# Performance work log

Hardware: AMD Instinct MI355X
Metric: run time of the kernel (lower is better)

Reference implementation:

```python
import jax, jax.numpy as jnp
import numpy as np

H = 512
V = 50000
S = 400
B = 64


def setup_inputs() -> dict:
    key = jax.random.key(0)
    ks = jax.random.split(key, 20)
    inp = {
        'input': jax.random.normal(ks[0], (1, B, H), jnp.float32),
        'encoder_states': jax.random.normal(ks[1], (S, B, H), jnp.float32),
        'oov_enc_mask': jax.random.randint(ks[2], (S, B), 0, 2, jnp.int32),
        'hidden': jnp.zeros((1, B, H), jnp.float32),
        # GRU params (PyTorch layout: gates ordered r, z, n)
        'W_ih': jax.random.normal(ks[3], (3 * H, H), jnp.float32) * 0.02,
        'W_hh': jax.random.normal(ks[4], (3 * H, H), jnp.float32) * 0.02,
        'b_ih': jax.random.normal(ks[5], (3 * H,), jnp.float32) * 0.02,
        'b_hh': jax.random.normal(ks[6], (3 * H,), jnp.float32) * 0.02,
        # output vocab projection Linear(2H, V)
        'out_W': jax.random.normal(ks[7], (V, 2 * H), jnp.float32) * 0.02,
        'out_b': jax.random.normal(ks[8], (V,), jnp.float32) * 0.02,
        # additive attention params
        'v': jax.random.normal(ks[9], (H, 1), jnp.float32) * 0.02,
        'Wh': jax.random.normal(ks[10], (H, H), jnp.float32) * 0.02,
        'Ws': jax.random.normal(ks[11], (H, H), jnp.float32) * 0.02,
        'b_attn': jax.random.normal(ks[12], (1, H), jnp.float32) * 0.02,
        # pointer probability Linears (H -> 1)
        'pWh': jax.random.normal(ks[13], (1, H), jnp.float32) * 0.02,
        'pWs': jax.random.normal(ks[14], (1, H), jnp.float32) * 0.02,
        'pWx': jax.random.normal(ks[15], (1, H), jnp.float32) * 0.02,
        'pWx_b': jax.random.normal(ks[16], (1,), jnp.float32) * 0.02,
    }
    return inp


def reference(input, encoder_states, oov_enc_mask, hidden,
              W_ih, W_hh, b_ih, b_hh, out_W, out_b,
              v, Wh, Ws, b_attn, pWh, pWs, pWx, pWx_b):
    x = input[0]            # (B, H)
    h0 = hidden[0]          # (B, H)

    # --- single-step GRU (PyTorch gate order r, z, n) ---
    gi = x @ W_ih.T + b_ih      # (B, 3H)
    gh = h0 @ W_hh.T + b_hh     # (B, 3H)
    ir, iz, inn = jnp.split(gi, 3, axis=1)
    hr, hz, hn = jnp.split(gh, 3, axis=1)
    r = jax.nn.sigmoid(ir + hr)
    z = jax.nn.sigmoid(iz + hz)
    n = jnp.tanh(inn + r * hn)
    h = (1.0 - z) * n + z * h0          # decoder_state, (B, H)
    hidden_new = h[None]                # (1, B, H)

    # --- Bahdanau additive attention, softmax over seq axis ---
    x1 = jnp.einsum('sbh,hk->sbk', encoder_states, Wh)   # (S, B, H)
    x2 = h @ Ws                                          # (B, H) broadcasts over S
    scores = jnp.squeeze(jnp.tanh(x1 + x2 + b_attn) @ v, 2)  # (S, B)
    attn = jax.nn.softmax(scores, axis=0)                # (S, B)
    attn_bs = attn.T                                     # (B, S)

    context = jnp.einsum('bs,sbh->bh', attn_bs, encoder_states)  # (B, H)
    global_state = jnp.concatenate([h, context], axis=1)         # (B, 2H)

    # --- pointer probability ---
    p = jax.nn.sigmoid(context @ pWh.T + h @ pWs.T + x @ pWx.T + pWx_b)  # (B, 1)

    vocab_distr = p * jax.nn.selu(global_state @ out_W.T + out_b)        # (B, V)
    oov_vocab_distr = (1.0 - p) * (attn_bs * oov_enc_mask.astype(jnp.float32).T)  # (B, S)
    extended_vocab_distr = jnp.concatenate([vocab_distr, oov_vocab_distr], axis=1)

    return extended_vocab_distr, hidden_new, jnp.squeeze(p), attn
```

## Files before the change

kernel.cpp:

```cpp
#include <hip/hip_runtime.h>
#include <cmath>

#define H    512
#define H2   1024
#define V    50000
#define SEQ  400
#define EXT  (V + SEQ)
#define NB_V 782

typedef __attribute__((ext_vector_type(8))) short short8;
typedef __attribute__((ext_vector_type(4))) float floatx4;

__device__ __forceinline__ unsigned int bfpack2(float lo, float hi) {
    unsigned int a = __float_as_uint(lo) + 0x8000u;
    unsigned int b = __float_as_uint(hi) + 0x8000u;
    return __builtin_amdgcn_perm(b, a, 0x07060302);
}
__device__ __forceinline__ uint4 pack8(float4 a, float4 b) {
    uint4 r;
    r.x = bfpack2(a.x, a.y);
    r.y = bfpack2(a.z, a.w);
    r.z = bfpack2(b.x, b.y);
    r.w = bfpack2(b.z, b.w);
    return r;
}
__device__ __forceinline__ float4 ld4(const float* p) { return *(const float4*)p; }

__global__ __launch_bounds__(256) void k01_fused(
    const float* __restrict__ x, const float* __restrict__ h0,
    const float* __restrict__ W_ih, const float* __restrict__ W_hh,
    float* __restrict__ gacc,
    const float* __restrict__ Wh, const float* __restrict__ Ws,
    unsigned short* __restrict__ WhT, unsigned short* __restrict__ WsT)
{
    __shared__ __align__(16) unsigned char smem[65536];
    const int tid = threadIdx.x;

    if (blockIdx.x >= 64) {
        float (*T)[65] = (float (*)[65])smem;
        const int e   = blockIdx.x - 64;
        const int zz  = e >> 6, rem = e & 63;
        const int k0  = (rem & 7) * 64, n0 = (rem >> 3) * 64;
        const float* src = zz ? Ws : Wh;
        unsigned short* dst = zz ? WsT : WhT;
        #pragma unroll
        for (int i = 0; i < 16; ++i) {
            int ee = i * 256 + tid;
            int r = ee >> 6, c = ee & 63;
            T[r][c] = src[(size_t)(k0 + r) * H + n0 + c];
        }
        __syncthreads();
        #pragma unroll
        for (int i = 0; i < 16; ++i) {
            int ee = i * 256 + tid;
            int nn = ee >> 6, kk = ee & 63;
            unsigned int u = __float_as_uint(T[kk][nn]) + 0x8000u;
            dst[(size_t)(n0 + nn) * H + k0 + kk] = (unsigned short)(u >> 16);
        }
        return;
    }

    uint4* Ax = (uint4*)smem;
    uint4* Ah = (uint4*)(smem + 8192);
    uint4 (*Bg)[512] = (uint4 (*)[512])(smem + 16384);
    const int wave = tid >> 6, lane = tid & 63;
    const int lrow = lane & 15, q = lane >> 4;
    const int jb = blockIdx.x & 7, ks = blockIdx.x >> 3;
    const int J0 = jb * 64;
    const int kc = ks * 64;

    #pragma unroll
    for (int c = 0; c < 2; ++c) {
        int idx = c * 256 + tid;
        int m = idx >> 3, j2 = idx & 7, k8 = j2 ^ (m & 7);
        const float* sx = x  + m * H + kc + k8 * 8;
        const float* sh = h0 + m * H + kc + k8 * 8;
        Ax[idx] = pack8(ld4(sx), ld4(sx + 4));
        Ah[idx] = pack8(ld4(sh), ld4(sh + 4));
    }
    #pragma unroll
    for (int g = 0; g < 6; ++g) {
        const float* Wb = (g < 3) ? W_ih : W_hh;
        const int go = (g % 3) * H;
        #pragma unroll
        for (int c = 0; c < 2; ++c) {
            int idx = c * 256 + tid;
            int n = idx >> 3, j2 = idx & 7, k8 = j2 ^ (n & 7);
            const float* sw = Wb + (size_t)(go + J0 + n) * H + kc + k8 * 8;
            Bg[g][idx] = pack8(ld4(sw), ld4(sw + 4));
        }
    }
    __syncthreads();

    floatx4 accm[6][4];
    #pragma unroll
    for (int g = 0; g < 6; ++g)
        #pragma unroll
        for (int mt = 0; mt < 4; ++mt) accm[g][mt] = (floatx4){0.f, 0.f, 0.f, 0.f};

    #pragma unroll
    for (int kk8 = 0; kk8 < 8; kk8 += 4) {
        const int k8 = kk8 + q;
        short8 ax[4], ah[4];
        #pragma unroll
        for (int mt = 0; mt < 4; ++mt) {
            int m = mt * 16 + lrow;
            ax[mt] = *(const short8*)&Ax[m * 8 + (k8 ^ (m & 7))];
            ah[mt] = *(const short8*)&Ah[m * 8 + (k8 ^ (m & 7))];
        }
        const int n = wave * 16 + lrow;
        const int gidx = n * 8 + (k8 ^ (n & 7));
        #pragma unroll
        for (int g = 0; g < 6; ++g) {
            short8 bb = *(const short8*)&Bg[g][gidx];
            #pragma unroll
            for (int mt = 0; mt < 4; ++mt)
                accm[g][mt] = __builtin_amdgcn_mfma_f32_16x16x32_bf16(
                    (g < 3) ? ax[mt] : ah[mt], bb, accm[g][mt], 0, 0, 0);
        }
    }
    const int j = J0 + wave * 16 + lrow;
    #pragma unroll
    for (int g = 0; g < 6; ++g)
        #pragma unroll
        for (int mt = 0; mt < 4; ++mt)
            #pragma unroll
            for (int r = 0; r < 4; ++r) {
                const int bb = mt * 16 + q * 4 + r;
                gacc[(((size_t)g * 8 + ks) * 64 + bb) * H + j] = accm[g][mt][r];
            }
}

__global__ __launch_bounds__(256) void k1_gru_fin(
    const float* __restrict__ gacc, const float* __restrict__ h0,
    const float* __restrict__ b_ih, const float* __restrict__ b_hh,
    float* __restrict__ h_out)
{
    const int e = blockIdx.x * 256 + threadIdx.x;
    const int j = e & (H - 1);
    const int b = e >> 9;
    float gs[6];
    #pragma unroll
    for (int g = 0; g < 6; ++g) {
        float sum = 0.f;
        #pragma unroll
        for (int ks = 0; ks < 8; ++ks)
            sum += gacc[(((size_t)g * 8 + ks) * 64 + b) * H + j];
        gs[g] = sum;
    }
    float rg = 1.f / (1.f + expf(-(gs[0] + b_ih[j] + gs[3] + b_hh[j])));
    float zg = 1.f / (1.f + expf(-(gs[1] + b_ih[H + j] + gs[4] + b_hh[H + j])));
    float ng = tanhf(gs[2] + b_ih[2 * H + j] + rg * (gs[5] + b_hh[2 * H + j]));
    float h0v = h0[b * H + j];
    h_out[b * H + j] = (1.f - zg) * ng + zg * h0v;
}

__global__ __launch_bounds__(256) void k2_x2(
    const float* __restrict__ h, const unsigned short* __restrict__ WsT,
    const float* __restrict__ b_attn, float* __restrict__ x2)
{
    __shared__ uint4 Ag[512];
    __shared__ uint4 Bgg[512];
    const int tid  = threadIdx.x;
    const int wave = tid >> 6, lane = tid & 63;
    const int lrow = lane & 15, q = lane >> 4;
    const int n0   = blockIdx.x * 64;

    floatx4 acc[4];
    #pragma unroll
    for (int mt = 0; mt < 4; ++mt) acc[mt] = (floatx4){0.f, 0.f, 0.f, 0.f};

    for (int kc = 0; kc < H; kc += 64) {
        __syncthreads();
        #pragma unroll
        for (int c = 0; c < 2; ++c) {
            int idx = c * 256 + tid;
            int m = idx >> 3, j2 = idx & 7, k8 = j2 ^ (m & 7);
            const float* sh = h + m * H + kc + k8 * 8;
            Ag[idx] = pack8(ld4(sh), ld4(sh + 4));
            Bgg[idx] = *(const uint4*)(WsT + (size_t)(n0 + m) * H + kc + k8 * 8);
        }
        __syncthreads();
        #pragma unroll
        for (int kk8 = 0; kk8 < 8; kk8 += 4) {
            const int k8 = kk8 + q;
            const int n = wave * 16 + lrow;
            short8 bb = *(const short8*)&Bgg[n * 8 + (k8 ^ (n & 7))];
            #pragma unroll
            for (int mt = 0; mt < 4; ++mt) {
                int m = mt * 16 + lrow;
                short8 a = *(const short8*)&Ag[m * 8 + (k8 ^ (m & 7))];
                acc[mt] = __builtin_amdgcn_mfma_f32_16x16x32_bf16(a, bb, acc[mt], 0, 0, 0);
            }
        }
    }
    const int n = n0 + wave * 16 + lrow;
    const float ba = b_attn[n];
    #pragma unroll
    for (int mt = 0; mt < 4; ++mt)
        #pragma unroll
        for (int r = 0; r < 4; ++r) {
            const int bb = mt * 16 + q * 4 + r;
            x2[bb * H + n] = acc[mt][r] + ba;
        }
}

__global__ __launch_bounds__(256) void k3_scores(
    const float* __restrict__ enc, const unsigned short* __restrict__ WhT,
    const float* __restrict__ x2, const float* __restrict__ v,
    float* __restrict__ part)
{
    __shared__ uint4 AsG[512];
    __shared__ uint4 BsG[4096];
    __shared__ float red[256];
    const int s    = blockIdx.x;
    const int tid  = threadIdx.x;
    const int wave = tid >> 6, lane = tid & 63;
    const int lrow = lane & 15, q = lane >> 4;

    floatx4 acc[4][8];
    #pragma unroll
    for (int mt = 0; mt < 4; ++mt)
        #pragma unroll
        for (int nt = 0; nt < 8; ++nt) acc[mt][nt] = (floatx4){0.f, 0.f, 0.f, 0.f};

    const float* Abase = enc + (size_t)s * 64 * H;
    for (int kc = 0; kc < H; kc += 64) {
        __syncthreads();
        #pragma unroll
        for (int c = 0; c < 2; ++c) {
            int idx = c * 256 + tid;
            int m = idx >> 3, k8 = (idx & 7) ^ (m & 7);
            const float* sa = Abase + m * H + kc + k8 * 8;
            AsG[idx] = pack8(ld4(sa), ld4(sa + 4));
        }
        #pragma unroll
        for (int c = 0; c < 16; ++c) {
            int idx = c * 256 + tid;
            int n = idx >> 3, k8 = (idx & 7) ^ (n & 7);
            BsG[idx] = *(const uint4*)(WhT + (size_t)n * H + kc + k8 * 8);
        }
        __syncthreads();
        #pragma unroll
        for (int kk8 = 0; kk8 < 8; kk8 += 4) {
            const int k8 = kk8 + q;
            short8 a[4];
            #pragma unroll
            for (int mt = 0; mt < 4; ++mt) {
                int m = mt * 16 + lrow;
                a[mt] = *(const short8*)&AsG[m * 8 + (k8 ^ (m & 7))];
            }
            #pragma unroll
            for (int nt = 0; nt < 8; ++nt) {
                int n = wave * 128 + nt * 16 + lrow;
                short8 bb = *(const short8*)&BsG[n * 8 + (k8 ^ (n & 7))];
                #pragma unroll
                for (int mt = 0; mt < 4; ++mt)
                    acc[mt][nt] = __builtin_amdgcn_mfma_f32_16x16x32_bf16(
                        a[mt], bb, acc[mt][nt], 0, 0, 0);
            }
        }
    }
    float val[4][4];
    #pragma unroll
    for (int mt = 0; mt < 4; ++mt) {
        #pragma unroll
        for (int r = 0; r < 4; ++r) {
            const int bb = mt * 16 + q * 4 + r;
            float sum = 0.f;
            #pragma unroll
            for (int nt = 0; nt < 8; ++nt) {
                const int n = wave * 128 + nt * 16 + lrow;
                sum += tanhf(acc[mt][nt][r] + x2[bb * H + n]) * v[n];
            }
            #pragma unroll
            for (int off = 8; off > 0; off >>= 1) sum += __shfl_down(sum, off, 16);
            val[mt][r] = sum;
        }
    }
    __syncthreads();
    if (lrow == 0) {
        #pragma unroll
        for (int mt = 0; mt < 4; ++mt)
            #pragma unroll
            for (int r = 0; r < 4; ++r)
                red[wave * 64 + mt * 16 + q * 4 + r] = val[mt][r];
    }
    __syncthreads();
    if (tid < 64) {
        float sc = red[tid] + red[64 + tid] + red[128 + tid] + red[192 + tid];
        part[(size_t)s * 64 + tid] = sc;
    }
}

__global__ __launch_bounds__(128) void k45_ctx(
    const float* __restrict__ part, const float* __restrict__ enc,
    float* __restrict__ attn_out, float* __restrict__ ctxp)
{
    const int b  = blockIdx.x;
    const int sg = blockIdx.y;
    const int t  = threadIdx.x;
    __shared__ float a_all[SEQ];
    __shared__ float red2[2];
    __shared__ float smax, ssum;

    float mv[4];
    float mx = -1e30f;
    #pragma unroll
    for (int i = 0; i < 4; ++i) {
        int s = i * 128 + t;
        if (s < SEQ) {
            float vv = part[(size_t)s * 64 + b];
            mv[i] = vv;
            mx = fmaxf(mx, vv);
        }
    }
    #pragma unroll
    for (int off = 32; off > 0; off >>= 1) mx = fmaxf(mx, __shfl_down(mx, off, 64));
    if ((t & 63) == 0) red2[t >> 6] = mx;
    __syncthreads();
    if (t == 0) smax = fmaxf(red2[0], red2[1]);
    __syncthreads();
    float ev[4];
    float se = 0.f;
    #pragma unroll
    for (int i = 0; i < 4; ++i) {
        int s = i * 128 + t;
        if (s < SEQ) { ev[i] = expf(mv[i] - smax); se += ev[i]; }
    }
    #pragma unroll
    for (int off = 32; off > 0; off >>= 1) se += __shfl_down(se, off, 64);
    if ((t & 63) == 0) red2[t >> 6] = se;
    __syncthreads();
    if (t == 0) ssum = red2[0] + red2[1];
    __syncthreads();
    const float inv = 1.f / ssum;
    #pragma unroll
    for (int i = 0; i < 4; ++i) {
        int s = i * 128 + t;
        if (s < SEQ) {
            float av = ev[i] * inv;
            a_all[s] = av;
            if (sg == 0) attn_out[s * 64 + b] = av;
        }
    }
    __syncthreads();

    const int hh = 4 * t;
    const float* p = enc + ((size_t)(sg * 50) * 64 + b) * H + hh;
    float4 a0 = {0.f, 0.f, 0.f, 0.f}, a1 = {0.f, 0.f, 0.f, 0.f};
    #pragma unroll 5
    for (int i = 0; i < 50; i += 2) {
        float4 e0 = *(const float4*)p;
        float4 e1 = *(const float4*)(p + (size_t)64 * H);
        float w0 = a_all[sg * 50 + i];
        float w1 = a_all[sg * 50 + i + 1];
        a0.x += w0 * e0.x; a0.y += w0 * e0.y; a0.z += w0 * e0.z; a0.w += w0 * e0.w;
        a1.x += w1 * e1.x; a1.y += w1 * e1.y; a1.z += w1 * e1.z; a1.w += w1 * e1.w;
        p += (size_t)128 * H;
    }
    float4 r;
    r.x = a0.x + a1.x; r.y = a0.y + a1.y; r.z = a0.z + a1.z; r.w = a0.w + a1.w;
    *(float4*)&ctxp[((size_t)sg * 64 + b) * H + hh] = r;
}

__global__ __launch_bounds__(512) void k5b_p(
    const float* __restrict__ ctxp, const float* __restrict__ pWh,
    const float* __restrict__ hdec, const float* __restrict__ pWs,
    const float* __restrict__ x, const float* __restrict__ pWx,
    const float* __restrict__ pWx_b,
    float* __restrict__ p_out, float* __restrict__ p_ws,
    unsigned short* __restrict__ gsb)
{
    const int b = blockIdx.x;
    const int t = threadIdx.x;
    __shared__ float rbuf[8];
    float c = 0.f;
    #pragma unroll
    for (int sg = 0; sg < 8; ++sg)
        c += ctxp[((size_t)sg * 64 + b) * H + t];
    float hv = hdec[b * H + t];
    gsb[(size_t)b * H2 + t]     = (unsigned short)((__float_as_uint(hv) + 0x8000u) >> 16);
    gsb[(size_t)b * H2 + H + t] = (unsigned short)((__float_as_uint(c)  + 0x8000u) >> 16);
    float term = c * pWh[t] + hv * pWs[t] + x[b * H + t] * pWx[t];
    #pragma unroll
    for (int off = 32; off > 0; off >>= 1) term += __shfl_down(term, off, 64);
    if ((t & 63) == 0) rbuf[t >> 6] = term;
    __syncthreads();
    if (t == 0) {
        float ssv = pWx_b[0];
        #pragma unroll
        for (int w = 0; w < 8; ++w) ssv += rbuf[w];
        float pv = 1.f / (1.f + expf(-ssv));
        p_out[b] = pv;
        p_ws[b]  = pv;
    }
}

__global__ __launch_bounds__(256) void k6_vocab(
    const unsigned short* __restrict__ gsb, const float* __restrict__ outW,
    const float* __restrict__ outb, const float* __restrict__ p_ws,
    const float* __restrict__ attn, const int* __restrict__ mask,
    float* __restrict__ ext)
{
    const int tid = threadIdx.x;
    if (blockIdx.x >= NB_V) {
        int e = (blockIdx.x - NB_V) * 256 + tid;
        int s = e >> 6, b = e & 63;
        float val = (1.f - p_ws[b]) * attn[e] * (mask[e] ? 1.f : 0.f);
        ext[(size_t)b * EXT + V + s] = val;
        return;
    }
    __shared__ uint4 AsG[512];
    __shared__ uint4 BsG[512];
    __shared__ float p_l[64];
    const int wave = tid >> 6, lane = tid & 63;
    const int lrow = lane & 15, q = lane >> 4;
    const int v0   = blockIdx.x * 64;

    if (tid < 64) p_l[tid] = p_ws[tid];

    floatx4 acc[4];
    #pragma unroll
    for (int mt = 0; mt < 4; ++mt) acc[mt] = (floatx4){0.f, 0.f, 0.f, 0.f};

    for (int kc = 0; kc < H2; kc += 64) {
        __syncthreads();
        #pragma unroll
        for (int c = 0; c < 2; ++c) {
            int idx = c * 256 + tid;
            int m = idx >> 3, k8 = (idx & 7) ^ (m & 7);
            AsG[idx] = *(const uint4*)(gsb + (size_t)m * H2 + kc + k8 * 8);
        }
        #pragma unroll
        for (int c = 0; c < 2; ++c) {
            int idx = c * 256 + tid;
            int n = idx >> 3, k8 = (idx & 7) ^ (n & 7);
            int vr = v0 + n; if (vr >= V) vr = V - 1;
            const float* sb = outW + (size_t)vr * H2 + kc + k8 * 8;
            BsG[idx] = pack8(ld4(sb), ld4(sb + 4));
        }
        __syncthreads();
        #pragma unroll
        for (int kk8 = 0; kk8 < 8; kk8 += 4) {
            const int k8 = kk8 + q;
            const int n = wave * 16 + lrow;
            short8 bb = *(const short8*)&BsG[n * 8 + (k8 ^ (n & 7))];
            #pragma unroll
            for (int mt = 0; mt < 4; ++mt) {
                int m = mt * 16 + lrow;
                short8 a = *(const short8*)&AsG[m * 8 + (k8 ^ (m & 7))];
                acc[mt] = __builtin_amdgcn_mfma_f32_16x16x32_bf16(a, bb, acc[mt], 0, 0, 0);
            }
        }
    }
    const int n = v0 + wave * 16 + lrow;
    if (n < V) {
        const float ob = outb[n];
        #pragma unroll
        for (int mt = 0; mt < 4; ++mt) {
            #pragma unroll
            for (int r = 0; r < 4; ++r) {
                const int bb = mt * 16 + q * 4 + r;
                float zz = acc[mt][r] + ob;
                float sv = (zz > 0.f) ? 1.0507009873554805f * zz
                                      : 1.7580993408473766f * (expf(zz) - 1.f);
                ext[(size_t)bb * EXT + n] = p_l[bb] * sv;
            }
        }
    }
}

extern "C" void kernel_launch(void* const* d_in, const int* in_sizes, int n_in,
                              void* d_out, int out_size, void* d_ws, size_t ws_size,
                              hipStream_t stream)
{
    (void)in_sizes; (void)n_in; (void)out_size; (void)ws_size;
    const float* x      = (const float*)d_in[0];
    const float* enc    = (const float*)d_in[1];
    const int*   mask   = (const int*)  d_in[2];
    const float* h0     = (const float*)d_in[3];
    const float* W_ih   = (const float*)d_in[4];
    const float* W_hh   = (const float*)d_in[5];
    const float* b_ih   = (const float*)d_in[6];
    const float* b_hh   = (const float*)d_in[7];
    const float* outW   = (const float*)d_in[8];
    const float* outb   = (const float*)d_in[9];
    const float* v      = (const float*)d_in[10];
    const float* Wh     = (const float*)d_in[11];
    const float* Ws     = (const float*)d_in[12];
    const float* b_attn = (const float*)d_in[13];
    const float* pWh    = (const float*)d_in[14];
    const float* pWs    = (const float*)d_in[15];
    const float* pWx    = (const float*)d_in[16];
    const float* pWx_b  = (const float*)d_in[17];

    float* out        = (float*)d_out;
    float* out_ext    = out;
    float* out_hidden = out + (size_t)64 * EXT;
    float* out_p      = out_hidden + 64 * H;
    float* out_attn   = out_p + 64;

    float* ws       = (float*)d_ws;
    float* ws_x2    = ws;
    float* ws_part  = ws_x2 + 64 * H;
    float* ws_ctxp  = ws_part + 4 * SEQ * 64;
    float* ws_p     = ws_ctxp + 8 * 64 * H;
    float* ws_gacc  = ws_p + 64;
    unsigned short* ws_whT = (unsigned short*)(ws_gacc + 6 * 8 * 64 * H);
    unsigned short* ws_wsT = ws_whT + (size_t)H * H;
    unsigned short* ws_gsb = ws_wsT + (size_t)H * H;

    k01_fused<<<192, 256, 0, stream>>>(x, h0, W_ih, W_hh, ws_gacc,
                                       Wh, Ws, ws_whT, ws_wsT);
    k1_gru_fin<<<128, 256, 0, stream>>>(ws_gacc, h0, b_ih, b_hh, out_hidden);
    k2_x2<<<8, 256, 0, stream>>>(out_hidden, ws_wsT, b_attn, ws_x2);
    k3_scores<<<SEQ, 256, 0, stream>>>(enc, ws_whT, ws_x2, v, ws_part);
    k45_ctx<<<dim3(64, 8), 128, 0, stream>>>(ws_part, enc, out_attn, ws_ctxp);
    k5b_p<<<64, 512, 0, stream>>>(ws_ctxp, pWh, out_hidden, pWs, x, pWx, pWx_b,
                                  out_p, ws_p, ws_gsb);
    k6_vocab<<<NB_V + 100, 256, 0, stream>>>(ws_gsb, outW, outb, ws_p,
                                             out_attn, mask, out_ext);
}
```

Baseline: 503.5 us.

## Keep encoder tile resident in LDS and loop N in quarters in scores kernel

The scores kernel now loads the whole 64x512 encoder slice once into shared memory as bf16, then sweeps the 512 output columns in four 128-column passes, streaming smaller Wh chunks per k-step. Each wave keeps only a 4x2 accumulator tile instead of 4x8, which cuts register pressure and may raise occupancy. LDS use changes from a large B buffer to a large A buffer, and the reduction scratch reuses the B buffer. The cost is more barriers per block and Wh being streamed in smaller pieces.

```diff
diff --git a/kernel.cpp b/kernel.cpp
--- a/kernel.cpp
+++ b/kernel.cpp
@@ -210,74 +210,88 @@
     const float* __restrict__ x2, const float* __restrict__ v,
     float* __restrict__ part)
 {
-    __shared__ uint4 AsG[512];
-    __shared__ uint4 BsG[4096];
-    __shared__ float red[256];
+    __shared__ uint4 AsG[4096];
+    __shared__ uint4 BsG[1024];
     const int s    = blockIdx.x;
     const int tid  = threadIdx.x;
     const int wave = tid >> 6, lane = tid & 63;
     const int lrow = lane & 15, q = lane >> 4;
 
-    floatx4 acc[4][8];
+    const float* Abase = enc + (size_t)s * 64 * H;
+    #pragma unroll
+    for (int c = 0; c < 16; ++c) {
+        int idx = c * 256 + tid;
+        int m = idx >> 6, kg = idx & 63;
+        const float* sa = Abase + m * H + kg * 8;
+        AsG[m * 64 + (kg ^ (m & 7))] = pack8(ld4(sa), ld4(sa + 4));
+    }
+
+    float val[4][4];
     #pragma unroll
     for (int mt = 0; mt < 4; ++mt)
         #pragma unroll
-        for (int nt = 0; nt < 8; ++nt) acc[mt][nt] = (floatx4){0.f, 0.f, 0.f, 0.f};
-
-    const float* Abase = enc + (size_t)s * 64 * H;
-    for (int kc = 0; kc < H; kc += 64) {
-        __syncthreads();
-        #pragma unroll
-        for (int c = 0; c < 2; ++c) {
-            int idx = c * 256 + tid;
-            int m = idx >> 3, k8 = (idx & 7) ^ (m & 7);
-            const float* sa = Abase + m * H + kc + k8 * 8;
-            AsG[idx] = pack8(ld4(sa), ld4(sa + 4));
-        }
-        #pragma unroll
-        for (int c = 0; c < 16; ++c) {
-            int idx = c * 256 + tid;
-            int n = idx >> 3, k8 = (idx & 7) ^ (n & 7);
-            BsG[idx] = *(const uint4*)(WhT + (size_t)n * H + kc + k8 * 8);
-        }
-        __syncthreads();
-        #pragma unroll
-        for (int kk8 = 0; kk8 < 8; kk8 += 4) {
-            const int k8 = kk8 + q;
-            short8 a[4];
-            #pragma unroll
-            for (int mt = 0; mt < 4; ++mt) {
-                int m = mt * 16 + lrow;
-                a[mt] = *(const short8*)&AsG[m * 8 + (k8 ^ (m & 7))];
-            }
-            #pragma unroll
-            for (int nt = 0; nt < 8; ++nt) {
-                int n = wave * 128 + nt * 16 + lrow;
-                short8 bb = *(const short8*)&BsG[n * 8 + (k8 ^ (n & 7))];
+        for (int r = 0; r < 4; ++r) val[mt][r] = 0.f;
+
+    for (int nq = 0; nq < 4; ++nq) {
+        const int n0 = nq * 128;
+        floatx4 acc[4][2];
+        #pragma unroll
+        for (int mt = 0; mt < 4; ++mt)
+            #pragma unroll
+            for (int nt = 0; nt < 2; ++nt) acc[mt][nt] = (floatx4){0.f, 0.f, 0.f, 0.f};
+
+        for (int kc = 0; kc < 8; ++kc) {
+            __syncthreads();
+            #pragma unroll
+            for (int c = 0; c < 4; ++c) {
+                int idx = c * 256 + tid;
+                int n = idx >> 3, k8 = (idx & 7) ^ (n & 7);
+                BsG[idx] = *(const uint4*)(WhT + (size_t)(n0 + n) * H + kc * 64 + k8 * 8);
+            }
+            __syncthreads();
+            #pragma unroll
+            for (int kk8 = 0; kk8 < 8; kk8 += 4) {
+                const int k8 = kk8 + q;
+                short8 a[4];
                 #pragma unroll
-                for (int mt = 0; mt < 4; ++mt)
-                    acc[mt][nt] = __builtin_amdgcn_mfma_f32_16x16x32_bf16(
-                        a[mt], bb, acc[mt][nt], 0, 0, 0);
-            }
-        }
-    }
-    float val[4][4];
-    #pragma unroll
-    for (int mt = 0; mt < 4; ++mt) {
+                for (int mt = 0; mt < 4; ++mt) {
+                    int m = mt * 16 + lrow;
+                    a[mt] = *(const short8*)&AsG[m * 64 + kc * 8 + (k8 ^ (m & 7))];
+                }
+                #pragma unroll
+                for (int nt = 0; nt < 2; ++nt) {
+                    int n = wave * 32 + nt * 16 + lrow;
+                    short8 bb = *(const short8*)&BsG[n * 8 + (k8 ^ (n & 7))];
+                    #pragma unroll
+                    for (int mt = 0; mt < 4; ++mt)
+                        acc[mt][nt] = __builtin_amdgcn_mfma_f32_16x16x32_bf16(
+                            a[mt], bb, acc[mt][nt], 0, 0, 0);
+                }
+            }
+        }
+        #pragma unroll
+        for (int mt = 0; mt < 4; ++mt)
+            #pragma unroll
+            for (int r = 0; r < 4; ++r) {
+                const int bb = mt * 16 + q * 4 + r;
+                #pragma unroll
+                for (int nt = 0; nt < 2; ++nt) {
+                    const int n = n0 + wave * 32 + nt * 16 + lrow;
+                    val[mt][r] += tanhf(acc[mt][nt][r] + x2[bb * H + n]) * v[n];
+                }
+            }
+    }
+
+    float* red = (float*)BsG;
+    #pragma unroll
+    for (int mt = 0; mt < 4; ++mt)
         #pragma unroll
         for (int r = 0; r < 4; ++r) {
-            const int bb = mt * 16 + q * 4 + r;
-            float sum = 0.f;
-            #pragma unroll
-            for (int nt = 0; nt < 8; ++nt) {
-                const int n = wave * 128 + nt * 16 + lrow;
-                sum += tanhf(acc[mt][nt][r] + x2[bb * H + n]) * v[n];
-            }
+            float sum = val[mt][r];
             #pragma unroll
             for (int off = 8; off > 0; off >>= 1) sum += __shfl_down(sum, off, 16);
             val[mt][r] = sum;
         }
-    }
     __syncthreads();
     if (lrow == 0) {
         #pragma unroll
```

New measurement: 453.9 us. -9.8%, faster.
